# Kernel optimization log

Measured on AMD Instinct MI355X. Metric: run time of the kernel, lower is better.

## Reference

```python
import jax, jax.numpy as jnp
import numpy as np

# config constants
B, L, ENC_IN = 8, 512, 7
D_MODEL = 768
EXPAND = 2
D_INNER = D_MODEL * EXPAND          # 1536
DT_RANK = (D_MODEL + 15) // 16      # 48
N_STATE = 16                         # configs.d_ff acts as SSM state size
K_CONV = 4
E_LAYERS = 2
C_OUT = 7
PRED_LEN = 96
EPS = 1e-5


def rmsnorm(x, w):
    return x * jax.lax.rsqrt(jnp.mean(x * x, axis=-1, keepdims=True) + EPS) * w


def silu(x):
    return x * jax.nn.sigmoid(x)


def positional_embedding(l, d):
    pos = np.arange(l, dtype=np.float32)[:, None]
    div = np.exp(np.arange(0, d, 2, dtype=np.float32) * (-np.log(10000.0) / d))
    pe = np.zeros((l, d), dtype=np.float32)
    pe[:, 0::2] = np.sin(pos * div)
    pe[:, 1::2] = np.cos(pos * div)
    return jnp.asarray(pe)


def causal_dwconv(x, w, b):
    # x: [b, d, l], w: [d, 1, k]; torch pads k-1 both sides then slices [:l] == left-pad k-1
    y = jax.lax.conv_general_dilated(
        x, w, window_strides=(1,), padding=[(K_CONV - 1, 0)],
        dimension_numbers=('NCH', 'OIH', 'NCH'), feature_group_count=D_INNER)
    return y + b[None, :, None]


def selective_scan(u, delta, A, Bm, Cm, Dp):
    # u, delta: [b,l,d]; A: [d,n]; Bm, Cm: [b,l,n]; Dp: [d]
    deltaA = jnp.exp(jnp.einsum('bld,dn->bldn', delta, A))          # [b,l,d,n]
    deltaBu = (delta * u)[..., None] * Bm[:, :, None, :]             # [b,l,d,n]

    def step(xc, inp):
        dA, dBu, Ct = inp                                            # [b,d,n],[b,d,n],[b,n]
        xc = dA * xc + dBu
        return xc, jnp.einsum('bdn,bn->bd', xc, Ct)

    b, l, d = u.shape
    x0 = jnp.zeros((b, d, A.shape[1]), u.dtype)
    _, ys = jax.lax.scan(step, x0, (jnp.moveaxis(deltaA, 1, 0),
                                    jnp.moveaxis(deltaBu, 1, 0),
                                    jnp.moveaxis(Cm, 1, 0)))
    y = jnp.moveaxis(ys, 0, 1)                                       # [b,l,d]
    return y + u * Dp


def mamba_block(x, in_w, conv_w, conv_b, xproj_w, dtproj_w, dtproj_b, A_log, Dp, outproj_w):
    xr = x @ in_w.T                                                  # [b,l,2*d_inner]
    xs, res = xr[..., :D_INNER], xr[..., D_INNER:]
    xs = causal_dwconv(jnp.swapaxes(xs, 1, 2), conv_w, conv_b)
    xs = silu(jnp.swapaxes(xs, 1, 2))
    # ssm
    A = -jnp.exp(A_log)
    x_dbl = xs @ xproj_w.T                                           # [b,l,dt_rank+2n]
    delta = x_dbl[..., :DT_RANK]
    Bm = x_dbl[..., DT_RANK:DT_RANK + N_STATE]
    Cm = x_dbl[..., DT_RANK + N_STATE:]
    delta = jax.nn.softplus(delta @ dtproj_w.T + dtproj_b)
    y = selective_scan(xs, delta, A, Bm, Cm, Dp)
    y = y * silu(res)
    return y @ outproj_w.T


def setup_inputs() -> dict:
    key = jax.random.key(0)
    ks = iter(jax.random.split(key, 32))
    s = 0.02
    d = {}
    d['x'] = jax.random.normal(next(ks), (B, L, ENC_IN), jnp.float32)
    d['token_w'] = jax.random.normal(next(ks), (D_MODEL, ENC_IN, 3), jnp.float32) * s
    d['time_w'] = jax.random.normal(next(ks), (D_MODEL, 1), jnp.float32) * s
    d['norm_w'] = jnp.ones((E_LAYERS, D_MODEL), jnp.float32)
    d['in_w'] = jax.random.normal(next(ks), (E_LAYERS, 2 * D_INNER, D_MODEL), jnp.float32) * s
    d['conv_w'] = jax.random.normal(next(ks), (E_LAYERS, D_INNER, 1, K_CONV), jnp.float32) * s
    d['conv_b'] = jnp.zeros((E_LAYERS, D_INNER), jnp.float32)
    d['xproj_w'] = jax.random.normal(next(ks), (E_LAYERS, DT_RANK + 2 * N_STATE, D_INNER), jnp.float32) * s
    d['dtproj_w'] = jax.random.normal(next(ks), (E_LAYERS, D_INNER, DT_RANK), jnp.float32) * s
    d['dtproj_b'] = jnp.zeros((E_LAYERS, D_INNER), jnp.float32)
    A = np.tile(np.arange(1, N_STATE + 1, dtype=np.float32)[None, :], (D_INNER, 1))
    d['A_log'] = jnp.tile(jnp.log(jnp.asarray(A))[None], (E_LAYERS, 1, 1))
    d['Dp'] = jnp.ones((E_LAYERS, D_INNER), jnp.float32)
    d['outproj_w'] = jax.random.normal(next(ks), (E_LAYERS, D_MODEL, D_INNER), jnp.float32) * s
    d['final_norm_w'] = jnp.ones((D_MODEL,), jnp.float32)
    d['out_w'] = jax.random.normal(next(ks), (C_OUT, D_MODEL), jnp.float32) * s
    return d


def reference(x, token_w, time_w, norm_w, in_w, conv_w, conv_b, xproj_w,
              dtproj_w, dtproj_b, A_log, Dp, outproj_w, final_norm_w, out_w):
    # instance normalization (mean/std detached)
    mean_enc = jax.lax.stop_gradient(jnp.mean(x, axis=1, keepdims=True))
    xc = x - mean_enc
    std_enc = jax.lax.stop_gradient(jnp.sqrt(jnp.var(xc, axis=1, keepdims=True) + 1e-5))
    xc = xc / std_enc
    # DataEmbedding: circular conv token emb + sinusoidal pos + timeF linear
    xp = jnp.pad(jnp.swapaxes(xc, 1, 2), ((0, 0), (0, 0), (1, 1)), mode='wrap')
    tok = jax.lax.conv_general_dilated(xp, token_w, (1,), 'VALID',
                                       dimension_numbers=('NCH', 'OIH', 'NCH'))
    tok = jnp.swapaxes(tok, 1, 2)                                    # [b,l,d_model]
    x_mark = (jnp.arange(L, dtype=x.dtype) / L)[None, :, None]       # [1,l,1]
    h = tok + positional_embedding(L, D_MODEL)[None] + x_mark @ time_w.T
    for e in range(E_LAYERS):
        h = mamba_block(rmsnorm(h, norm_w[e]), in_w[e], conv_w[e], conv_b[e],
                        xproj_w[e], dtproj_w[e], dtproj_b[e], A_log[e], Dp[e],
                        outproj_w[e]) + h
    h = rmsnorm(h, final_norm_w)
    out = h @ out_w.T
    out = out * std_enc + mean_enc
    return out[:, -PRED_LEN:, :]
```

## Files before the change

kernel.cpp:

```cpp
#include <hip/hip_runtime.h>
#include <hip/hip_bf16.h>
#include <math.h>

#define BSZ 8
#define LSEQ 512
#define ENC_IN 7
#define D_MODEL 768
#define D_INNER 1536
#define DT_RANK 48
#define N_STATE 16
#define K_CONV 4
#define E_LAYERS 2
#define C_OUT 7
#define PRED_LEN 96
#define EPSV 1e-5f
#define XN 80
#define KSPLIT 4

#define ROWS (BSZ*LSEQ)
#define NC 16
#define CL (LSEQ/NC)
#define NTILE (LSEQ/16)
#define LOG2E 1.44269504088896f

typedef __bf16 bf16x8 __attribute__((ext_vector_type(8)));
typedef float  f32x4  __attribute__((ext_vector_type(4)));

__device__ __forceinline__ float fexp2(float x) {
    float r;
    asm("v_exp_f32 %0, %1" : "=v"(r) : "v"(x));
    return r;
}
__device__ __forceinline__ float softplusf(float v) {
    return fmaxf(v, 0.f) + log1pf(__expf(-fabsf(v)));
}
__device__ __forceinline__ void glds16(const char* g, char* l) {
    __builtin_amdgcn_global_load_lds((const __attribute__((address_space(1))) unsigned int*)g,
                                     (__attribute__((address_space(3))) unsigned int*)l, 16, 0, 0);
}

__device__ __forceinline__ float block_sum(float v, float* tmp) {
    #pragma unroll
    for (int off = 32; off > 0; off >>= 1) v += __shfl_down(v, off);
    int lane = threadIdx.x & 63, wid = threadIdx.x >> 6;
    __syncthreads();
    if (lane == 0) tmp[wid] = v;
    __syncthreads();
    return tmp[0] + tmp[1] + tmp[2] + tmp[3];
}

__global__ __launch_bounds__(256) void cvt_all(const float* __restrict__ in_w,
                                               const float* __restrict__ outw,
                                               const float* __restrict__ xpw,
                                               const float* __restrict__ dtw,
                                               __hip_bfloat16* __restrict__ inw_bf,
                                               __hip_bfloat16* __restrict__ outw_bf,
                                               __hip_bfloat16* __restrict__ xpw_bf,
                                               __hip_bfloat16* __restrict__ dtw_bf) {
    const int N1 = E_LAYERS*2*D_INNER*D_MODEL;
    const int N2 = E_LAYERS*D_MODEL*D_INNER;
    const int N3 = E_LAYERS*XN*D_INNER;
    const int N4 = E_LAYERS*D_INNER*64;
    int i = blockIdx.x*256 + threadIdx.x;
    if (i < N1) {
        inw_bf[i] = __float2bfloat16(in_w[i]);
    } else if (i < N1+N2) {
        int j = i - N1; outw_bf[j] = __float2bfloat16(outw[j]);
    } else if (i < N1+N2+N3) {
        int j = i - N1 - N2; xpw_bf[j] = __float2bfloat16(xpw[j]);
    } else if (i < N1+N2+N3+N4) {
        int j = i - N1 - N2 - N3;
        int r = j >> 6, c = j & 63;
        dtw_bf[j] = __float2bfloat16(c < DT_RANK ? dtw[r*DT_RANK + c] : 0.f);
    }
}

__global__ __launch_bounds__(256) void stats_kernel(const float* __restrict__ x,
                                                    float* __restrict__ mean,
                                                    float* __restrict__ stdv) {
    int bc = blockIdx.x;
    int b = bc / ENC_IN, c = bc % ENC_IN;
    __shared__ float tmp[4];
    float s = 0.f, sq = 0.f;
    for (int l = threadIdx.x; l < LSEQ; l += 256) {
        float v = x[((size_t)(b*LSEQ + l))*ENC_IN + c];
        s += v; sq += v*v;
    }
    s = block_sum(s, tmp);
    sq = block_sum(sq, tmp);
    if (threadIdx.x == 0) {
        float m = s / LSEQ;
        float var = sq / LSEQ - m*m;
        if (var < 0.f) var = 0.f;
        mean[bc] = m;
        stdv[bc] = sqrtf(var + EPSV);
    }
}

__global__ __launch_bounds__(256) void embed_kernel(const float* __restrict__ x,
                                                    const float* __restrict__ token_w,
                                                    const float* __restrict__ time_w,
                                                    const float* __restrict__ mean,
                                                    const float* __restrict__ stdv,
                                                    float* __restrict__ h) {
    int bl = blockIdx.x;
    int b = bl >> 9, l = bl & 511;
    __shared__ float sxc[ENC_IN*3];
    if (threadIdx.x < ENC_IN*3) {
        int c = threadIdx.x / 3, k = threadIdx.x % 3;
        int lk = (l + k - 1) & 511;
        float v = x[((size_t)(b*LSEQ + lk))*ENC_IN + c];
        sxc[threadIdx.x] = (v - mean[b*ENC_IN + c]) / stdv[b*ENC_IN + c];
    }
    __syncthreads();
    #pragma unroll
    for (int i = 0; i < 3; i++) {
        int d = threadIdx.x + i*256;
        float acc = 0.f;
        const float* w = token_w + (size_t)d*21;
        #pragma unroll
        for (int t = 0; t < 21; t++) acc += sxc[t] * w[t];
        int d2 = d & ~1;
        float div = __expf((float)d2 * (-9.210340371976184f / (float)D_MODEL));
        float ang = (float)l * div;
        float pe = (d & 1) ? cosf(ang) : sinf(ang);
        float tm = ((float)l / (float)LSEQ) * time_w[d];
        h[(size_t)bl*D_MODEL + d] = acc + pe + tm;
    }
}

__global__ __launch_bounds__(256) void rmsnorm_bf16(const float* __restrict__ h,
                                                    const float* __restrict__ w,
                                                    __hip_bfloat16* __restrict__ xn) {
    size_t base = (size_t)blockIdx.x * D_MODEL;
    __shared__ float tmp[4];
    float ss = 0.f;
    for (int k = threadIdx.x; k < D_MODEL; k += 256) { float v = h[base+k]; ss += v*v; }
    ss = block_sum(ss, tmp);
    float inv = rsqrtf(ss / (float)D_MODEL + EPSV);
    for (int k = threadIdx.x; k < D_MODEL; k += 256)
        xn[base+k] = __float2bfloat16(h[base+k]*inv*w[k]);
}

__global__ __launch_bounds__(256) void gemm_inproj(const __hip_bfloat16* __restrict__ A,
                                                   const __hip_bfloat16* __restrict__ Bw,
                                                   __hip_bfloat16* __restrict__ Cxs,
                                                   __hip_bfloat16* __restrict__ Cg) {
    __shared__ __align__(16) __hip_bfloat16 As[3][128*32];
    __shared__ __align__(16) __hip_bfloat16 Bs[3][128*32];
    const int K = D_MODEL;
    const int NK = K/32;
    int tid = threadIdx.x, lane = tid & 63, w = tid >> 6;
    int gx = gridDim.x;
    int nwg = gx * gridDim.y;
    int orig = blockIdx.y*gx + blockIdx.x;
    int swz = (orig & 7)*(nwg >> 3) + (orig >> 3);
    int m0 = (swz / gx) * 128, n0 = (swz % gx) * 128;
    int wr = w >> 1, wc = w & 1;
    int kq = lane >> 4, rr = lane & 15;

    f32x4 acc[4][4];
    #pragma unroll
    for (int i = 0; i < 4; i++)
        #pragma unroll
        for (int j = 0; j < 4; j++) acc[i][j] = (f32x4){0.f,0.f,0.f,0.f};

    const char* Ab = (const char*)A;
    const char* Bb = (const char*)Bw;
    char* AsB = (char*)As;
    char* BsB = (char*)Bs;

    int c0 = tid, c1 = tid + 256;
    int r0 = c0 >> 2, q0 = (c0 & 3) ^ ((r0 >> 1) & 3);
    int r1 = c1 >> 2, q1 = (c1 & 3) ^ ((r1 >> 1) & 3);
    int sw = (kq ^ ((rr >> 1) & 3)) * 16;

    auto stage = [&](int buf, int kt) {
        int k0 = kt*32;
        glds16(Ab + ((size_t)(m0+r0)*K + k0 + q0*8)*2, AsB + buf*8192 + c0*16);
        glds16(Ab + ((size_t)(m0+r1)*K + k0 + q1*8)*2, AsB + buf*8192 + c1*16);
        glds16(Bb + ((size_t)(n0+r0)*K + k0 + q0*8)*2, BsB + buf*8192 + c0*16);
        glds16(Bb + ((size_t)(n0+r1)*K + k0 + q1*8)*2, BsB + buf*8192 + c1*16);
    };

    stage(0, 0);
    stage(1, 1);

    for (int k = 0; k < NK; k++) {
        int cur = k % 3;
        __builtin_amdgcn_s_barrier();
        if (k + 2 < NK) stage((k + 2) % 3, k + 2);
        asm volatile("s_waitcnt vmcnt(8)" ::: "memory");
        __builtin_amdgcn_s_barrier();
        bf16x8 af[4], bfr[4];
        #pragma unroll
        for (int mi = 0; mi < 4; mi++) af[mi]  = *(const bf16x8*)(AsB + cur*8192 + (wr*64 + mi*16 + rr)*64 + sw);
        #pragma unroll
        for (int ni = 0; ni < 4; ni++) bfr[ni] = *(const bf16x8*)(BsB + cur*8192 + (wc*64 + ni*16 + rr)*64 + sw);
        #pragma unroll
        for (int mi = 0; mi < 4; mi++)
            #pragma unroll
            for (int ni = 0; ni < 4; ni++)
                acc[mi][ni] = __builtin_amdgcn_mfma_f32_16x16x32_bf16(af[mi], bfr[ni], acc[mi][ni], 0, 0, 0);
    }

    #pragma unroll
    for (int mi = 0; mi < 4; mi++) {
        #pragma unroll
        for (int ni = 0; ni < 4; ni++) {
            int row0 = m0 + wr*64 + mi*16;
            int col  = n0 + wc*64 + ni*16 + rr;
            if (col >= D_INNER) {
                __hip_bfloat16 g4[4];
                #pragma unroll
                for (int r = 0; r < 4; r++) {
                    float v = acc[mi][ni][r];
                    g4[r] = __float2bfloat16(v / (1.f + __expf(-v)));
                }
                int cd = col - D_INNER;
                *(uint2*)&Cg[((size_t)(row0 >> 4)*D_INNER + cd)*16 + kq*4] = *(uint2*)g4;
            } else {
                #pragma unroll
                for (int r = 0; r < 4; r++) {
                    int row = row0 + kq*4 + r;
                    Cxs[(size_t)row*D_INNER + col] = __float2bfloat16(acc[mi][ni][r]);
                }
            }
        }
    }
}

__global__ __launch_bounds__(256) void gemm_dtproj(const float* __restrict__ P,
                                                   const __hip_bfloat16* __restrict__ Bw,
                                                   const float* __restrict__ bias,
                                                   float* __restrict__ xdbl,
                                                   __hip_bfloat16* __restrict__ delta) {
    __shared__ __align__(16) __hip_bfloat16 As[128*64];
    __shared__ __align__(16) __hip_bfloat16 Bs[128*64];
    const int K = 64;
    int tid = threadIdx.x, lane = tid & 63, w = tid >> 6;
    int gx = gridDim.x;
    int nwg = gx * gridDim.y;
    int orig = blockIdx.y*gx + blockIdx.x;
    int swz = (orig & 7)*(nwg >> 3) + (orig >> 3);
    int m0 = (swz / gx) * 128, n0 = (swz % gx) * 128;
    int wr = w >> 1, wc = w & 1;
    int kq = lane >> 4, rr = lane & 15;

    f32x4 acc[4][4];
    #pragma unroll
    for (int i = 0; i < 4; i++)
        #pragma unroll
        for (int j = 0; j < 4; j++) acc[i][j] = (f32x4){0.f,0.f,0.f,0.f};

    const char* Bb = (const char*)Bw;
    char* AsB = (char*)As;
    char* BsB = (char*)Bs;

    #pragma unroll
    for (int c = 0; c < 4; c++) {
        int idx = c*256 + tid;
        int r = idx >> 3, q = idx & 7;
        int qs = q ^ (r & 7);
        glds16(Bb + ((size_t)(n0+r)*K + qs*8)*2, BsB + idx*16);
    }

    const size_t RX = (size_t)ROWS*XN;
    #pragma unroll
    for (int it = 0; it < 2; it++) {
        int idx = it*1024 + tid;
        if (idx < 128*10) {
            int row = idx / 10, ch = idx % 10;
            const float* p0 = P + (size_t)(m0+row)*XN + ch*8;
            f32x4 a0 = *(const f32x4*)(p0)      + *(const f32x4*)(p0+RX)
                     + *(const f32x4*)(p0+2*RX) + *(const f32x4*)(p0+3*RX);
            f32x4 a1 = *(const f32x4*)(p0+4)        + *(const f32x4*)(p0+RX+4)
                     + *(const f32x4*)(p0+2*RX+4)   + *(const f32x4*)(p0+3*RX+4);
            if (n0 == 0) {
                float* xd = xdbl + (size_t)(m0+row)*XN + ch*8;
                *(f32x4*)(xd)   = a0;
                *(f32x4*)(xd+4) = a1;
            }
            if (ch < 8) {
                bf16x8 hv;
                if (ch < 6) {
                    #pragma unroll
                    for (int j = 0; j < 4; j++) { hv[j] = (__bf16)a0[j]; hv[4+j] = (__bf16)a1[j]; }
                } else {
                    bf16x8 z = {}; hv = z;
                }
                *(bf16x8*)(AsB + row*128 + ((ch ^ (row & 7))*16)) = hv;
            }
        }
    }
    __syncthreads();

    #pragma unroll
    for (int kh = 0; kh < 2; kh++) {
        int ch = ((kh*4 + kq) ^ (rr & 7)) * 16;
        bf16x8 af[4], bfr[4];
        #pragma unroll
        for (int mi = 0; mi < 4; mi++) af[mi]  = *(const bf16x8*)(AsB + (wr*64 + mi*16 + rr)*128 + ch);
        #pragma unroll
        for (int ni = 0; ni < 4; ni++) bfr[ni] = *(const bf16x8*)(BsB + (wc*64 + ni*16 + rr)*128 + ch);
        #pragma unroll
        for (int mi = 0; mi < 4; mi++)
            #pragma unroll
            for (int ni = 0; ni < 4; ni++)
                acc[mi][ni] = __builtin_amdgcn_mfma_f32_16x16x32_bf16(af[mi], bfr[ni], acc[mi][ni], 0, 0, 0);
    }

    #pragma unroll
    for (int mi = 0; mi < 4; mi++) {
        #pragma unroll
        for (int ni = 0; ni < 4; ni++) {
            int row0 = m0 + wr*64 + mi*16;
            int col  = n0 + wc*64 + ni*16 + rr;
            __hip_bfloat16 d4[4];
            #pragma unroll
            for (int r = 0; r < 4; r++) {
                float v = acc[mi][ni][r] + bias[col];
                d4[r] = __float2bfloat16(softplusf(v));
            }
            *(uint2*)&delta[((size_t)(row0 >> 4)*D_INNER + col)*16 + kq*4] = *(uint2*)d4;
        }
    }
}

__global__ __launch_bounds__(256) void gemm_outproj(const __hip_bfloat16* __restrict__ A,
                                                    const __hip_bfloat16* __restrict__ Bw,
                                                    float* __restrict__ C) {
    __shared__ __align__(16) __hip_bfloat16 As[3][128*32];
    __shared__ __align__(16) __hip_bfloat16 Bs[3][64*32];
    int tid = threadIdx.x, lane = tid & 63, w = tid >> 6;
    int gx = gridDim.x;
    int nwg = gx * gridDim.y;
    int orig = blockIdx.y*gx + blockIdx.x;
    int swz = (orig & 7)*(nwg >> 3) + (orig >> 3);
    int m0 = (swz / gx) * 128, n0 = (swz % gx) * 64;
    int wr = w >> 1, wc = w & 1;
    int kq = lane >> 4, rr = lane & 15;
    const int K = D_INNER;
    const int NK = K/32;

    f32x4 acc[4][2];
    #pragma unroll
    for (int i = 0; i < 4; i++)
        #pragma unroll
        for (int j = 0; j < 2; j++) acc[i][j] = (f32x4){0.f,0.f,0.f,0.f};

    const char* Ab = (const char*)A;
    const char* Bb = (const char*)Bw;
    char* AsB = (char*)As;
    char* BsB = (char*)Bs;

    int cA0 = tid, cA1 = tid + 256;
    int rA0 = cA0 >> 2, qA0 = (cA0 & 3) ^ ((rA0 >> 1) & 3);
    int rA1 = cA1 >> 2, qA1 = (cA1 & 3) ^ ((rA1 >> 1) & 3);
    int rB = tid >> 2,  qB  = (tid & 3) ^ ((rB >> 1) & 3);
    int sw = (kq ^ ((rr >> 1) & 3)) * 16;

    auto stage = [&](int buf, int kt) {
        int k0 = kt*32;
        glds16(Ab + ((size_t)(m0+rA0)*K + k0 + qA0*8)*2, AsB + buf*8192 + cA0*16);
        glds16(Ab + ((size_t)(m0+rA1)*K + k0 + qA1*8)*2, AsB + buf*8192 + cA1*16);
        glds16(Bb + ((size_t)(n0+rB)*K + k0 + qB*8)*2,  BsB + buf*4096 + tid*16);
    };

    stage(0, 0);
    stage(1, 1);

    for (int k = 0; k < NK; k++) {
        int cur = k % 3;
        __builtin_amdgcn_s_barrier();
        if (k + 2 < NK) stage((k + 2) % 3, k + 2);
        asm volatile("s_waitcnt vmcnt(6)" ::: "memory");
        __builtin_amdgcn_s_barrier();
        bf16x8 af[4], bfr[2];
        #pragma unroll
        for (int mi = 0; mi < 4; mi++) af[mi]  = *(const bf16x8*)(AsB + cur*8192 + (wr*64 + mi*16 + rr)*64 + sw);
        #pragma unroll
        for (int ni = 0; ni < 2; ni++) bfr[ni] = *(const bf16x8*)(BsB + cur*4096 + (wc*32 + ni*16 + rr)*64 + sw);
        #pragma unroll
        for (int mi = 0; mi < 4; mi++)
            #pragma unroll
            for (int ni = 0; ni < 2; ni++)
                acc[mi][ni] = __builtin_amdgcn_mfma_f32_16x16x32_bf16(af[mi], bfr[ni], acc[mi][ni], 0, 0, 0);
    }

    #pragma unroll
    for (int mi = 0; mi < 4; mi++) {
        #pragma unroll
        for (int ni = 0; ni < 2; ni++) {
            #pragma unroll
            for (int r = 0; r < 4; r++) {
                int row = m0 + wr*64 + mi*16 + kq*4 + r;
                int col = n0 + wc*32 + ni*16 + rr;
                size_t o = (size_t)row*D_MODEL + col;
                C[o] = acc[mi][ni][r] + C[o];
            }
        }
    }
}

__global__ __launch_bounds__(256) void gemm_xproj(const __hip_bfloat16* __restrict__ A,
                                                  const __hip_bfloat16* __restrict__ W,
                                                  float* __restrict__ P) {
    __shared__ __align__(16) __hip_bfloat16 As[3][64*64];
    __shared__ __align__(16) __hip_bfloat16 Bs[3][96*64];
    int tid = threadIdx.x, lane = tid & 63, w = tid >> 6;
    int m0 = blockIdx.x * 64;
    int k0 = blockIdx.y * (D_INNER / KSPLIT);
    int kq = lane >> 4, rr = lane & 15;
    const int NK = (D_INNER/KSPLIT)/64;
    f32x4 acc[5];
    #pragma unroll
    for (int i = 0; i < 5; i++) acc[i] = (f32x4){0.f,0.f,0.f,0.f};
    const char* Ab = (const char*)A;
    const char* Wb = (const char*)W;
    char* AsB = (char*)As;
    char* BsB = (char*)Bs;

    auto stage = [&](int buf, int it) {
        int kk = k0 + it*64;
        #pragma unroll
        for (int cA = 0; cA < 2; cA++) {
            int idx = cA*256 + tid;
            int r = idx >> 3, q = (idx & 7) ^ (r & 7);
            glds16(Ab + ((size_t)(m0+r)*D_INNER + kk + q*8)*2, AsB + buf*8192 + idx*16);
        }
        #pragma unroll
        for (int cB = 0; cB < 3; cB++) {
            int idx = cB*256 + tid;
            int r = idx >> 3, q = (idx & 7) ^ (r & 7);
            int rs = r < XN ? r : XN-1;
            glds16(Wb + ((size_t)rs*D_INNER + kk + q*8)*2, BsB + buf*12288 + idx*16);
        }
    };

    stage(0, 0);
    stage(1, 1);

    for (int it = 0; it < NK; it++) {
        int cur = it % 3;
        __builtin_amdgcn_s_barrier();
        if (it + 2 < NK) stage((it + 2) % 3, it + 2);
        asm volatile("s_waitcnt vmcnt(10)" ::: "memory");
        __builtin_amdgcn_s_barrier();
        #pragma unroll
        for (int kh = 0; kh < 2; kh++) {
            bf16x8 a = *(const bf16x8*)(AsB + cur*8192 + (w*16 + rr)*128 + (((kh*4 + kq) ^ (rr & 7)))*16);
            #pragma unroll
            for (int ni = 0; ni < 5; ni++) {
                bf16x8 b = *(const bf16x8*)(BsB + cur*12288 + (ni*16 + rr)*128 + (((kh*4 + kq) ^ (rr & 7)))*16);
                acc[ni] = __builtin_amdgcn_mfma_f32_16x16x32_bf16(a, b, acc[ni], 0, 0, 0);
            }
        }
    }
    float* Cp = P + (size_t)blockIdx.y * ROWS * XN;
    #pragma unroll
    for (int ni = 0; ni < 5; ni++)
        #pragma unroll
        for (int r = 0; r < 4; r++) {
            int row = m0 + w*16 + kq*4 + r;
            int col = ni*16 + rr;
            Cp[(size_t)row*XN + col] = acc[ni][r];
        }
}

__global__ __launch_bounds__(256) void dwconv_silu(const __hip_bfloat16* __restrict__ xs,
                                                   const float* __restrict__ cw,
                                                   const float* __restrict__ cb,
                                                   __hip_bfloat16* __restrict__ u_bf) {
    int idx = blockIdx.x*256 + threadIdx.x;
    int dg = idx % (D_INNER/8);
    int t  = idx / (D_INNER/8);
    if (t >= ROWS) return;
    int d0 = dg*8;
    int l = t & 511, b = t >> 9;
    bf16x8 rows[K_CONV];
    #pragma unroll
    for (int k = 0; k < K_CONV; k++) {
        int ll = l - (K_CONV-1) + k;
        if (ll >= 0) rows[k] = *(const bf16x8*)(xs + ((size_t)(b*LSEQ + ll))*D_INNER + d0);
        else { bf16x8 z = {}; rows[k] = z; }
    }
    bf16x8 outv;
    #pragma unroll
    for (int j = 0; j < 8; j++) {
        int d = d0 + j;
        const float4 w4 = *(const float4*)(cw + d*K_CONV);
        float acc = cb[d]
                  + (float)rows[0][j]*w4.x + (float)rows[1][j]*w4.y
                  + (float)rows[2][j]*w4.z + (float)rows[3][j]*w4.w;
        float v = acc / (1.f + __expf(-acc));
        outv[j] = (__bf16)v;
    }
    *(bf16x8*)(u_bf + (size_t)t*D_INNER + d0) = outv;
}

__global__ __launch_bounds__(256) void scan_p1(const __hip_bfloat16* __restrict__ u,
                                               const __hip_bfloat16* __restrict__ delta_blk,
                                               const float* __restrict__ xdbl,
                                               const float* __restrict__ A_log,
                                               float* __restrict__ xfin,
                                               float* __restrict__ sumdlt) {
    int d = blockIdx.x*256 + threadIdx.x;
    int c = blockIdx.y, b = blockIdx.z;
    int l0 = c*CL;
    const float* al = A_log + d*N_STATE;
    bool fast = true;
    #pragma unroll
    for (int n = 0; n < N_STATE; n++)
        fast = fast && (fabsf(__expf(al[n]) - (float)(n+1)) < 1e-3f);
    float xs[N_STATE];
    #pragma unroll
    for (int n = 0; n < N_STATE; n++) xs[n] = 0.f;
    const __hip_bfloat16* pu = u + (size_t)(b*LSEQ + l0)*D_INNER + d;
    const float* pB = xdbl + (size_t)(b*LSEQ + l0)*XN + DT_RANK;
    float sd = 0.f;
    if (fast) {
        #pragma unroll
        for (int tt = 0; tt < 2; tt++) {
            const __hip_bfloat16* db = delta_blk + ((size_t)(b*NTILE + (l0>>4) + tt)*D_INNER + d)*16;
            bf16x8 d0 = *(const bf16x8*)db;
            bf16x8 d1 = *(const bf16x8*)(db + 8);
            #pragma unroll
            for (int i = 0; i < 16; i++) {
                float dlt = (float)(i < 8 ? d0[i] : d1[i-8]);
                float uu = __bfloat162float(*pu); pu += D_INNER;
                float du = dlt*uu;
                sd += dlt;
                float e1 = fexp2(-dlt*LOG2E);
                float e = e1;
                xs[0] = e*xs[0] + du*pB[0];
                #pragma unroll
                for (int n = 1; n < N_STATE; n++) {
                    e *= e1;
                    xs[n] = e*xs[n] + du*pB[n];
                }
                pB += XN;
            }
        }
    } else {
        #pragma unroll
        for (int tt = 0; tt < 2; tt++) {
            const __hip_bfloat16* db = delta_blk + ((size_t)(b*NTILE + (l0>>4) + tt)*D_INNER + d)*16;
            bf16x8 d0 = *(const bf16x8*)db;
            bf16x8 d1 = *(const bf16x8*)(db + 8);
            #pragma unroll
            for (int i = 0; i < 16; i++) {
                float dlt = (float)(i < 8 ? d0[i] : d1[i-8]);
                float uu = __bfloat162float(*pu); pu += D_INNER;
                float du = dlt*uu;
                sd += dlt;
                #pragma unroll
                for (int n = 0; n < N_STATE; n++) {
                    float A2n = -__expf(al[n]) * LOG2E;
                    xs[n] = fexp2(dlt*A2n)*xs[n] + du*pB[n];
                }
                pB += XN;
            }
        }
    }
    float* px = xfin + (size_t)((b*NC + c)*N_STATE)*D_INNER + d;
    #pragma unroll
    for (int n = 0; n < N_STATE; n++) px[n*D_INNER] = xs[n];
    sumdlt[(size_t)(b*NC + c)*D_INNER + d] = sd;
}

__global__ __launch_bounds__(256) void scan_p2(float* __restrict__ xfin,
                                               const float* __restrict__ sumdlt,
                                               const float* __restrict__ A_log) {
    int idx = blockIdx.x*256 + threadIdx.x;
    int d = idx % D_INNER;
    int r = idx / D_INNER;
    int n = r & 15;
    int b = r >> 4;
    float A2 = -__expf(A_log[d*N_STATE + n]) * LOG2E;
    float cr = 0.f;
    for (int c = 1; c < NC; c++) {
        size_t jp = (size_t)(b*NC + c - 1);
        float xf = xfin[(jp*N_STATE + n)*D_INNER + d];
        float s  = sumdlt[jp*D_INNER + d];
        cr = fexp2(A2 * s) * cr + xf;
        xfin[(jp*N_STATE + n)*D_INNER + d] = cr;
    }
}

__global__ __launch_bounds__(256) void scan_p3(const __hip_bfloat16* __restrict__ u,
                                               const __hip_bfloat16* __restrict__ delta_blk,
                                               const __hip_bfloat16* __restrict__ gres,
                                               const float* __restrict__ xdbl,
                                               const float* __restrict__ A_log,
                                               const float* __restrict__ Dp,
                                               const float* __restrict__ carry,
                                               __hip_bfloat16* __restrict__ ygate) {
    int d = blockIdx.x*256 + threadIdx.x;
    int c = blockIdx.y, b = blockIdx.z;
    int l0 = c*CL;
    const float* al = A_log + d*N_STATE;
    bool fast = true;
    #pragma unroll
    for (int n = 0; n < N_STATE; n++)
        fast = fast && (fabsf(__expf(al[n]) - (float)(n+1)) < 1e-3f);
    float xs[N_STATE];
    if (c == 0) {
        #pragma unroll
        for (int n = 0; n < N_STATE; n++) xs[n] = 0.f;
    } else {
        const float* pc = carry + (size_t)((b*NC + c - 1)*N_STATE)*D_INNER + d;
        #pragma unroll
        for (int n = 0; n < N_STATE; n++) xs[n] = pc[n*D_INNER];
    }
    float Dv = Dp[d];
    const __hip_bfloat16* pu = u + (size_t)(b*LSEQ + l0)*D_INNER + d;
    const float* pB = xdbl + (size_t)(b*LSEQ + l0)*XN + DT_RANK;
    __hip_bfloat16* py = ygate + (size_t)(b*LSEQ + l0)*D_INNER + d;
    if (fast) {
        #pragma unroll
        for (int tt = 0; tt < 2; tt++) {
            size_t tb = (size_t)(b*NTILE + (l0>>4) + tt)*D_INNER + d;
            const __hip_bfloat16* db = delta_blk + tb*16;
            bf16x8 d0 = *(const bf16x8*)db;
            bf16x8 d1 = *(const bf16x8*)(db + 8);
            const __hip_bfloat16* gb = gres + tb*16;
            bf16x8 g0 = *(const bf16x8*)gb;
            bf16x8 g1 = *(const bf16x8*)(gb + 8);
            #pragma unroll
            for (int i = 0; i < 16; i++) {
                float dlt = (float)(i < 8 ? d0[i] : d1[i-8]);
                float gr  = (float)(i < 8 ? g0[i] : g1[i-8]);
                float uu = __bfloat162float(*pu); pu += D_INNER;
                float du = dlt*uu;
                float e1 = fexp2(-dlt*LOG2E);
                float e = e1;
                float acc;
                xs[0] = e*xs[0] + du*pB[0];
                acc = xs[0]*pB[N_STATE + 0];
                #pragma unroll
                for (int n = 1; n < N_STATE; n++) {
                    e *= e1;
                    xs[n] = e*xs[n] + du*pB[n];
                    acc += xs[n]*pB[N_STATE + n];
                }
                pB += XN;
                float y = acc + uu*Dv;
                *py = __float2bfloat16(y * gr); py += D_INNER;
            }
        }
    } else {
        #pragma unroll
        for (int tt = 0; tt < 2; tt++) {
            size_t tb = (size_t)(b*NTILE + (l0>>4) + tt)*D_INNER + d;
            const __hip_bfloat16* db = delta_blk + tb*16;
            bf16x8 d0 = *(const bf16x8*)db;
            bf16x8 d1 = *(const bf16x8*)(db + 8);
            const __hip_bfloat16* gb = gres + tb*16;
            bf16x8 g0 = *(const bf16x8*)gb;
            bf16x8 g1 = *(const bf16x8*)(gb + 8);
            #pragma unroll
            for (int i = 0; i < 16; i++) {
                float dlt = (float)(i < 8 ? d0[i] : d1[i-8]);
                float gr  = (float)(i < 8 ? g0[i] : g1[i-8]);
                float uu = __bfloat162float(*pu); pu += D_INNER;
                float du = dlt*uu;
                float acc = 0.f;
                #pragma unroll
                for (int n = 0; n < N_STATE; n++) {
                    float A2n = -__expf(al[n]) * LOG2E;
                    xs[n] = fexp2(dlt*A2n)*xs[n] + du*pB[n];
                    acc += xs[n]*pB[N_STATE + n];
                }
                pB += XN;
                float y = acc + uu*Dv;
                *py = __float2bfloat16(y * gr); py += D_INNER;
            }
        }
    }
}

__global__ __launch_bounds__(256) void final_kernel(const float* __restrict__ h,
                                                    const float* __restrict__ fnw,
                                                    const float* __restrict__ out_w,
                                                    const float* __restrict__ mean,
                                                    const float* __restrict__ stdv,
                                                    float* __restrict__ out) {
    int bid = blockIdx.x;
    int b = bid / PRED_LEN, lo = bid % PRED_LEN;
    int l = LSEQ - PRED_LEN + lo;
    const float* row = h + ((size_t)(b*LSEQ + l))*D_MODEL;
    __shared__ float tmp[4];
    float ss = 0.f;
    for (int k = threadIdx.x; k < D_MODEL; k += 256) { float v = row[k]; ss += v*v; }
    ss = block_sum(ss, tmp);
    float inv = rsqrtf(ss / (float)D_MODEL + EPSV);
    float acc[C_OUT] = {};
    for (int k = threadIdx.x; k < D_MODEL; k += 256) {
        float hn = row[k]*fnw[k];
        #pragma unroll
        for (int c = 0; c < C_OUT; c++) acc[c] += hn*out_w[c*D_MODEL + k];
    }
    #pragma unroll
    for (int c = 0; c < C_OUT; c++) {
        float s = block_sum(acc[c], tmp);
        if (threadIdx.x == 0)
            out[((size_t)(b*PRED_LEN + lo))*C_OUT + c] = s*inv*stdv[b*ENC_IN + c] + mean[b*ENC_IN + c];
    }
}

extern "C" void kernel_launch(void* const* d_in, const int* in_sizes, int n_in,
                              void* d_out, int out_size, void* d_ws, size_t ws_size,
                              hipStream_t stream) {
    const float* x        = (const float*)d_in[0];
    const float* token_w  = (const float*)d_in[1];
    const float* time_w   = (const float*)d_in[2];
    const float* norm_w   = (const float*)d_in[3];
    const float* in_w     = (const float*)d_in[4];
    const float* conv_w   = (const float*)d_in[5];
    const float* conv_b   = (const float*)d_in[6];
    const float* xproj_w  = (const float*)d_in[7];
    const float* dtproj_w = (const float*)d_in[8];
    const float* dtproj_b = (const float*)d_in[9];
    const float* A_log    = (const float*)d_in[10];
    const float* Dp       = (const float*)d_in[11];
    const float* outproj_w= (const float*)d_in[12];
    const float* final_nw = (const float*)d_in[13];
    const float* out_w    = (const float*)d_in[14];
    float* out = (float*)d_out;

    float* ws   = (float*)d_ws;
    float* mean = ws;
    float* stdv = ws + 64;
    float* h    = ws + 128;
    float* xdbl = h    + (size_t)ROWS*D_MODEL;
    float* sumd = xdbl + (size_t)ROWS*XN;
    float* xfin = sumd + (size_t)BSZ*NC*D_INNER;
    float* pout = xfin + (size_t)BSZ*NC*D_INNER*N_STATE;
    float* fend = pout + (size_t)KSPLIT*ROWS*XN;
    __hip_bfloat16* xn_bf  = (__hip_bfloat16*)fend;
    __hip_bfloat16* xs_bf  = xn_bf + (size_t)ROWS*D_MODEL;
    __hip_bfloat16* u_bf   = xs_bf + (size_t)ROWS*D_INNER;
    __hip_bfloat16* gres   = u_bf  + (size_t)ROWS*D_INNER;
    __hip_bfloat16* ygate  = gres  + (size_t)ROWS*D_INNER;
    __hip_bfloat16* delta  = ygate + (size_t)ROWS*D_INNER;
    __hip_bfloat16* inw_bf = delta + (size_t)ROWS*D_INNER;
    __hip_bfloat16* outw_bf= inw_bf + (size_t)E_LAYERS*2*D_INNER*D_MODEL;
    __hip_bfloat16* xpw_bf = outw_bf+ (size_t)E_LAYERS*D_MODEL*D_INNER;
    __hip_bfloat16* dtw_bf = xpw_bf + (size_t)E_LAYERS*XN*D_INNER;

    {
        const int NT = E_LAYERS*2*D_INNER*D_MODEL + E_LAYERS*D_MODEL*D_INNER
                     + E_LAYERS*XN*D_INNER + E_LAYERS*D_INNER*64;
        cvt_all<<<(NT+255)/256, 256, 0, stream>>>(in_w, outproj_w, xproj_w, dtproj_w,
                                                  inw_bf, outw_bf, xpw_bf, dtw_bf);
    }

    stats_kernel<<<BSZ*ENC_IN, 256, 0, stream>>>(x, mean, stdv);
    embed_kernel<<<ROWS, 256, 0, stream>>>(x, token_w, time_w, mean, stdv, h);

    for (int e = 0; e < E_LAYERS; e++) {
        rmsnorm_bf16<<<ROWS, 256, 0, stream>>>(h, norm_w + e*D_MODEL, xn_bf);
        gemm_inproj<<<dim3(2*D_INNER/128, ROWS/128), 256, 0, stream>>>(
            xn_bf, inw_bf + (size_t)e*2*D_INNER*D_MODEL, xs_bf, gres);
        dwconv_silu<<<(ROWS*(D_INNER/8) + 255)/256, 256, 0, stream>>>(
            xs_bf, conv_w + (size_t)e*D_INNER*K_CONV, conv_b + e*D_INNER, u_bf);
        gemm_xproj<<<dim3(ROWS/64, KSPLIT), 256, 0, stream>>>(
            u_bf, xpw_bf + (size_t)e*XN*D_INNER, pout);
        gemm_dtproj<<<dim3(D_INNER/128, ROWS/128), 256, 0, stream>>>(
            pout, dtw_bf + (size_t)e*D_INNER*64, dtproj_b + e*D_INNER, xdbl, delta);
        const float* Alog_e = A_log + (size_t)e*D_INNER*N_STATE;
        scan_p1<<<dim3(D_INNER/256, NC, BSZ), 256, 0, stream>>>(
            u_bf, delta, xdbl, Alog_e, xfin, sumd);
        scan_p2<<<(BSZ*D_INNER*N_STATE)/256, 256, 0, stream>>>(
            xfin, sumd, Alog_e);
        scan_p3<<<dim3(D_INNER/256, NC, BSZ), 256, 0, stream>>>(
            u_bf, delta, gres, xdbl, Alog_e, Dp + (size_t)e*D_INNER, xfin, ygate);
        gemm_outproj<<<dim3(D_MODEL/64, ROWS/128), 256, 0, stream>>>(
            ygate, outw_bf + (size_t)e*D_MODEL*D_INNER, h);
    }

    final_kernel<<<BSZ*PRED_LEN, 256, 0, stream>>>(h, final_nw, out_w, mean, stdv, out);
}
```

Before: 376.4 us.

## Widen in-proj tiles, split-K out-proj with atomics, vectorize rmsnorm

The in-projection GEMM tile grows from 128x128 to 128x256, which doubles per-wave MFMA work and halves the grid. The out-projection moves to 128x128 tiles with a split-K of 2 over a z-dimension and accumulates into the residual with atomicAdd. The K-loops use tail-aware vmcnt waits and s_setprio around the MFMA blocks, and rmsnorm now does one f32x4 load per thread. Risks include higher register pressure from the 4x8 accumulators, atomic contention and nondeterministic summation order in out-proj, and fewer workgroups for in-proj.

```diff
diff --git a/kernel.cpp b/kernel.cpp
--- a/kernel.cpp
+++ b/kernel.cpp
@@ -134,20 +134,27 @@
                                                     __hip_bfloat16* __restrict__ xn) {
     size_t base = (size_t)blockIdx.x * D_MODEL;
     __shared__ float tmp[4];
-    float ss = 0.f;
-    for (int k = threadIdx.x; k < D_MODEL; k += 256) { float v = h[base+k]; ss += v*v; }
+    int tid = threadIdx.x;
+    f32x4 v = {0.f,0.f,0.f,0.f};
+    if (tid < 192) v = *(const f32x4*)(h + base + tid*4);
+    float ss = v[0]*v[0] + v[1]*v[1] + v[2]*v[2] + v[3]*v[3];
     ss = block_sum(ss, tmp);
     float inv = rsqrtf(ss / (float)D_MODEL + EPSV);
-    for (int k = threadIdx.x; k < D_MODEL; k += 256)
-        xn[base+k] = __float2bfloat16(h[base+k]*inv*w[k]);
-}
-
-__global__ __launch_bounds__(256) void gemm_inproj(const __hip_bfloat16* __restrict__ A,
-                                                   const __hip_bfloat16* __restrict__ Bw,
-                                                   __hip_bfloat16* __restrict__ Cxs,
-                                                   __hip_bfloat16* __restrict__ Cg) {
+    if (tid < 192) {
+        f32x4 wv = *(const f32x4*)(w + tid*4);
+        __hip_bfloat16 o4[4];
+        #pragma unroll
+        for (int j = 0; j < 4; j++) o4[j] = __float2bfloat16(v[j]*inv*wv[j]);
+        *(uint2*)(xn + base + tid*4) = *(uint2*)o4;
+    }
+}
+
+__global__ __launch_bounds__(256, 2) void gemm_inproj(const __hip_bfloat16* __restrict__ A,
+                                                      const __hip_bfloat16* __restrict__ Bw,
+                                                      __hip_bfloat16* __restrict__ Cxs,
+                                                      __hip_bfloat16* __restrict__ Cg) {
     __shared__ __align__(16) __hip_bfloat16 As[3][128*32];
-    __shared__ __align__(16) __hip_bfloat16 Bs[3][128*32];
+    __shared__ __align__(16) __hip_bfloat16 Bs[3][256*32];
     const int K = D_MODEL;
     const int NK = K/32;
     int tid = threadIdx.x, lane = tid & 63, w = tid >> 6;
@@ -155,32 +162,36 @@
     int nwg = gx * gridDim.y;
     int orig = blockIdx.y*gx + blockIdx.x;
     int swz = (orig & 7)*(nwg >> 3) + (orig >> 3);
-    int m0 = (swz / gx) * 128, n0 = (swz % gx) * 128;
+    int m0 = (swz / gx) * 128, n0 = (swz % gx) * 256;
     int wr = w >> 1, wc = w & 1;
     int kq = lane >> 4, rr = lane & 15;
 
-    f32x4 acc[4][4];
+    f32x4 acc[4][8];
     #pragma unroll
     for (int i = 0; i < 4; i++)
         #pragma unroll
-        for (int j = 0; j < 4; j++) acc[i][j] = (f32x4){0.f,0.f,0.f,0.f};
+        for (int j = 0; j < 8; j++) acc[i][j] = (f32x4){0.f,0.f,0.f,0.f};
 
     const char* Ab = (const char*)A;
     const char* Bb = (const char*)Bw;
     char* AsB = (char*)As;
     char* BsB = (char*)Bs;
 
-    int c0 = tid, c1 = tid + 256;
-    int r0 = c0 >> 2, q0 = (c0 & 3) ^ ((r0 >> 1) & 3);
-    int r1 = c1 >> 2, q1 = (c1 & 3) ^ ((r1 >> 1) & 3);
+    int cA0 = tid, cA1 = tid + 256;
+    int rA0 = cA0 >> 2, qA0 = (cA0 & 3) ^ ((rA0 >> 1) & 3);
+    int rA1 = cA1 >> 2, qA1 = (cA1 & 3) ^ ((rA1 >> 1) & 3);
     int sw = (kq ^ ((rr >> 1) & 3)) * 16;
 
     auto stage = [&](int buf, int kt) {
         int k0 = kt*32;
-        glds16(Ab + ((size_t)(m0+r0)*K + k0 + q0*8)*2, AsB + buf*8192 + c0*16);
-        glds16(Ab + ((size_t)(m0+r1)*K + k0 + q1*8)*2, AsB + buf*8192 + c1*16);
-        glds16(Bb + ((size_t)(n0+r0)*K + k0 + q0*8)*2, BsB + buf*8192 + c0*16);
-        glds16(Bb + ((size_t)(n0+r1)*K + k0 + q1*8)*2, BsB + buf*8192 + c1*16);
+        glds16(Ab + ((size_t)(m0+rA0)*K + k0 + qA0*8)*2, AsB + buf*8192 + cA0*16);
+        glds16(Ab + ((size_t)(m0+rA1)*K + k0 + qA1*8)*2, AsB + buf*8192 + cA1*16);
+        #pragma unroll
+        for (int j = 0; j < 4; j++) {
+            int idx = j*256 + tid;
+            int r = idx >> 2, q = (idx & 3) ^ ((r >> 1) & 3);
+            glds16(Bb + ((size_t)(n0+r)*K + k0 + q*8)*2, BsB + buf*16384 + idx*16);
+        }
     };
 
     stage(0, 0);
@@ -190,26 +201,30 @@
         int cur = k % 3;
         __builtin_amdgcn_s_barrier();
         if (k + 2 < NK) stage((k + 2) % 3, k + 2);
-        asm volatile("s_waitcnt vmcnt(8)" ::: "memory");
+        if (k + 2 < NK)      asm volatile("s_waitcnt vmcnt(12)" ::: "memory");
+        else if (k + 1 < NK) asm volatile("s_waitcnt vmcnt(6)" ::: "memory");
+        else                 asm volatile("s_waitcnt vmcnt(0)" ::: "memory");
         __builtin_amdgcn_s_barrier();
-        bf16x8 af[4], bfr[4];
-        #pragma unroll
-        for (int mi = 0; mi < 4; mi++) af[mi]  = *(const bf16x8*)(AsB + cur*8192 + (wr*64 + mi*16 + rr)*64 + sw);
-        #pragma unroll
-        for (int ni = 0; ni < 4; ni++) bfr[ni] = *(const bf16x8*)(BsB + cur*8192 + (wc*64 + ni*16 + rr)*64 + sw);
+        bf16x8 af[4], bfr[8];
+        #pragma unroll
+        for (int mi = 0; mi < 4; mi++) af[mi]  = *(const bf16x8*)(AsB + cur*8192  + (wr*64 + mi*16 + rr)*64 + sw);
+        #pragma unroll
+        for (int ni = 0; ni < 8; ni++) bfr[ni] = *(const bf16x8*)(BsB + cur*16384 + (wc*128 + ni*16 + rr)*64 + sw);
+        __builtin_amdgcn_s_setprio(1);
         #pragma unroll
         for (int mi = 0; mi < 4; mi++)
             #pragma unroll
-            for (int ni = 0; ni < 4; ni++)
+            for (int ni = 0; ni < 8; ni++)
                 acc[mi][ni] = __builtin_amdgcn_mfma_f32_16x16x32_bf16(af[mi], bfr[ni], acc[mi][ni], 0, 0, 0);
+        __builtin_amdgcn_s_setprio(0);
     }
 
     #pragma unroll
     for (int mi = 0; mi < 4; mi++) {
         #pragma unroll
-        for (int ni = 0; ni < 4; ni++) {
+        for (int ni = 0; ni < 8; ni++) {
             int row0 = m0 + wr*64 + mi*16;
-            int col  = n0 + wc*64 + ni*16 + rr;
+            int col  = n0 + wc*128 + ni*16 + rr;
             if (col >= D_INNER) {
                 __hip_bfloat16 g4[4];
                 #pragma unroll
@@ -331,40 +346,41 @@
                                                     const __hip_bfloat16* __restrict__ Bw,
                                                     float* __restrict__ C) {
     __shared__ __align__(16) __hip_bfloat16 As[3][128*32];
-    __shared__ __align__(16) __hip_bfloat16 Bs[3][64*32];
+    __shared__ __align__(16) __hip_bfloat16 Bs[3][128*32];
     int tid = threadIdx.x, lane = tid & 63, w = tid >> 6;
     int gx = gridDim.x;
     int nwg = gx * gridDim.y;
     int orig = blockIdx.y*gx + blockIdx.x;
     int swz = (orig & 7)*(nwg >> 3) + (orig >> 3);
-    int m0 = (swz / gx) * 128, n0 = (swz % gx) * 64;
+    int m0 = (swz / gx) * 128, n0 = (swz % gx) * 128;
     int wr = w >> 1, wc = w & 1;
     int kq = lane >> 4, rr = lane & 15;
     const int K = D_INNER;
-    const int NK = K/32;
-
-    f32x4 acc[4][2];
+    const int kbase = blockIdx.z * (D_INNER/2);
+    const int NK = (D_INNER/2)/32;
+
+    f32x4 acc[4][4];
     #pragma unroll
     for (int i = 0; i < 4; i++)
         #pragma unroll
-        for (int j = 0; j < 2; j++) acc[i][j] = (f32x4){0.f,0.f,0.f,0.f};
+        for (int j = 0; j < 4; j++) acc[i][j] = (f32x4){0.f,0.f,0.f,0.f};
 
     const char* Ab = (const char*)A;
     const char* Bb = (const char*)Bw;
     char* AsB = (char*)As;
     char* BsB = (char*)Bs;
 
-    int cA0 = tid, cA1 = tid + 256;
-    int rA0 = cA0 >> 2, qA0 = (cA0 & 3) ^ ((rA0 >> 1) & 3);
-    int rA1 = cA1 >> 2, qA1 = (cA1 & 3) ^ ((rA1 >> 1) & 3);
-    int rB = tid >> 2,  qB  = (tid & 3) ^ ((rB >> 1) & 3);
+    int c0 = tid, c1 = tid + 256;
+    int r0 = c0 >> 2, q0 = (c0 & 3) ^ ((r0 >> 1) & 3);
+    int r1 = c1 >> 2, q1 = (c1 & 3) ^ ((r1 >> 1) & 3);
     int sw = (kq ^ ((rr >> 1) & 3)) * 16;
 
     auto stage = [&](int buf, int kt) {
-        int k0 = kt*32;
-        glds16(Ab + ((size_t)(m0+rA0)*K + k0 + qA0*8)*2, AsB + buf*8192 + cA0*16);
-        glds16(Ab + ((size_t)(m0+rA1)*K + k0 + qA1*8)*2, AsB + buf*8192 + cA1*16);
-        glds16(Bb + ((size_t)(n0+rB)*K + k0 + qB*8)*2,  BsB + buf*4096 + tid*16);
+        int k0 = kbase + kt*32;
+        glds16(Ab + ((size_t)(m0+r0)*K + k0 + q0*8)*2, AsB + buf*8192 + c0*16);
+        glds16(Ab + ((size_t)(m0+r1)*K + k0 + q1*8)*2, AsB + buf*8192 + c1*16);
+        glds16(Bb + ((size_t)(n0+r0)*K + k0 + q0*8)*2, BsB + buf*8192 + c0*16);
+        glds16(Bb + ((size_t)(n0+r1)*K + k0 + q1*8)*2, BsB + buf*8192 + c1*16);
     };
 
     stage(0, 0);
@@ -374,30 +390,33 @@
         int cur = k % 3;
         __builtin_amdgcn_s_barrier();
         if (k + 2 < NK) stage((k + 2) % 3, k + 2);
-        asm volatile("s_waitcnt vmcnt(6)" ::: "memory");
+        if (k + 2 < NK)      asm volatile("s_waitcnt vmcnt(8)" ::: "memory");
+        else if (k + 1 < NK) asm volatile("s_waitcnt vmcnt(4)" ::: "memory");
+        else                 asm volatile("s_waitcnt vmcnt(0)" ::: "memory");
         __builtin_amdgcn_s_barrier();
-        bf16x8 af[4], bfr[2];
+        bf16x8 af[4], bfr[4];
         #pragma unroll
         for (int mi = 0; mi < 4; mi++) af[mi]  = *(const bf16x8*)(AsB + cur*8192 + (wr*64 + mi*16 + rr)*64 + sw);
         #pragma unroll
-        for (int ni = 0; ni < 2; ni++) bfr[ni] = *(const bf16x8*)(BsB + cur*4096 + (wc*32 + ni*16 + rr)*64 + sw);
+        for (int ni = 0; ni < 4; ni++) bfr[ni] = *(const bf16x8*)(BsB + cur*8192 + (wc*64 + ni*16 + rr)*64 + sw);
+        __builtin_amdgcn_s_setprio(1);
         #pragma unroll
         for (int mi = 0; mi < 4; mi++)
             #pragma unroll
-            for (int ni = 0; ni < 2; ni++)
+            for (int ni = 0; ni < 4; ni++)
                 acc[mi][ni] = __builtin_amdgcn_mfma_f32_16x16x32_bf16(af[mi], bfr[ni], acc[mi][ni], 0, 0, 0);
+        __builtin_amdgcn_s_setprio(0);
     }
 
     #pragma unroll
     for (int mi = 0; mi < 4; mi++) {
         #pragma unroll
-        for (int ni = 0; ni < 2; ni++) {
+        for (int ni = 0; ni < 4; ni++) {
             #pragma unroll
             for (int r = 0; r < 4; r++) {
                 int row = m0 + wr*64 + mi*16 + kq*4 + r;
-                int col = n0 + wc*32 + ni*16 + rr;
-                size_t o = (size_t)row*D_MODEL + col;
-                C[o] = acc[mi][ni][r] + C[o];
+                int col = n0 + wc*64 + ni*16 + rr;
+                atomicAdd(&C[(size_t)row*D_MODEL + col], acc[mi][ni][r]);
             }
         }
     }
@@ -445,7 +464,9 @@
         int cur = it % 3;
         __builtin_amdgcn_s_barrier();
         if (it + 2 < NK) stage((it + 2) % 3, it + 2);
-        asm volatile("s_waitcnt vmcnt(10)" ::: "memory");
+        if (it + 2 < NK)      asm volatile("s_waitcnt vmcnt(10)" ::: "memory");
+        else if (it + 1 < NK) asm volatile("s_waitcnt vmcnt(5)" ::: "memory");
+        else                  asm volatile("s_waitcnt vmcnt(0)" ::: "memory");
         __builtin_amdgcn_s_barrier();
         #pragma unroll
         for (int kh = 0; kh < 2; kh++) {
@@ -761,7 +782,7 @@
 
     for (int e = 0; e < E_LAYERS; e++) {
         rmsnorm_bf16<<<ROWS, 256, 0, stream>>>(h, norm_w + e*D_MODEL, xn_bf);
-        gemm_inproj<<<dim3(2*D_INNER/128, ROWS/128), 256, 0, stream>>>(
+        gemm_inproj<<<dim3(2*D_INNER/256, ROWS/128), 256, 0, stream>>>(
             xn_bf, inw_bf + (size_t)e*2*D_INNER*D_MODEL, xs_bf, gres);
         dwconv_silu<<<(ROWS*(D_INNER/8) + 255)/256, 256, 0, stream>>>(
             xs_bf, conv_w + (size_t)e*D_INNER*K_CONV, conv_b + e*D_INNER, u_bf);
@@ -776,7 +797,7 @@
             xfin, sumd, Alog_e);
         scan_p3<<<dim3(D_INNER/256, NC, BSZ), 256, 0, stream>>>(
             u_bf, delta, gres, xdbl, Alog_e, Dp + (size_t)e*D_INNER, xfin, ygate);
-        gemm_outproj<<<dim3(D_MODEL/64, ROWS/128), 256, 0, stream>>>(
+        gemm_outproj<<<dim3(D_MODEL/128, ROWS/128, 2), 256, 0, stream>>>(
             ygate, outw_bf + (size_t)e*D_MODEL*D_INNER, h);
     }
 
```

Result: slower. 401.3 us (+6.6%).
